# Optimization experiments

Hardware: AMD Instinct MI355X
Metric: run time of the kernel (lower is better)

The kernel has to match this reference:

```python
import jax, jax.numpy as jnp
import numpy as np

NUM_HEADS = 16
NUM_KV_HEADS = 4
HEAD_DIM = 128
TOP_K = 4
RMS_EPS = 1e-6
ROPE_THETA = 10000.0


def setup_inputs() -> dict:
    key = jax.random.key(0)
    ks = jax.random.split(key, 10)
    T, h, E, I, SI = 1024, 2048, 16, 512, 1024
    s = 0.02  # weight init scale for numerical sanity
    return {
        "hidden_states": jax.random.normal(ks[0], (T, h), jnp.float32),
        "residual": jax.random.normal(ks[1], (T, h), jnp.float32),
        "rms1_w": jnp.ones((h,), jnp.float32),
        "rms2_w": jnp.ones((h,), jnp.float32),
        "w_qkv": jax.random.normal(ks[2], (h, NUM_HEADS * HEAD_DIM + 2 * NUM_KV_HEADS * HEAD_DIM), jnp.float32) * s,
        "w_dense": jax.random.normal(ks[3], (NUM_HEADS * HEAD_DIM, h), jnp.float32) * s,
        "gate_w": jax.random.normal(ks[4], (h, E), jnp.float32) * s,
        "w13": jax.random.normal(ks[5], (E, h, 2 * I), jnp.float32) * s,
        "w2": jax.random.normal(ks[6], (E, I, h), jnp.float32) * s,
        "sw13": jax.random.normal(ks[7], (h, 2 * SI), jnp.float32) * s,
        "sw2": jax.random.normal(ks[8], (SI, h), jnp.float32) * s,
        "position_ids": jnp.arange(T, dtype=jnp.int32),
    }


def _rmsnorm(x, w, eps=RMS_EPS):
    var = jnp.mean(jnp.square(x), axis=-1, keepdims=True)
    return x * jax.lax.rsqrt(var + eps) * w


def _rope_neox(pos, x):
    # x: [T, H, D]; rotate-half (neox) style over full head_dim
    d = x.shape[-1]
    inv_freq = 1.0 / (ROPE_THETA ** (jnp.arange(0, d, 2, dtype=jnp.float32) / d))  # [d/2]
    ang = pos.astype(jnp.float32)[:, None] * inv_freq  # [T, d/2]
    cos = jnp.cos(ang)[:, None, :]  # [T, 1, d/2]
    sin = jnp.sin(ang)[:, None, :]
    x1, x2 = x[..., : d // 2], x[..., d // 2 :]
    return jnp.concatenate([x1 * cos - x2 * sin, x2 * cos + x1 * sin], axis=-1)


def reference(hidden_states, residual, rms1_w, rms2_w, w_qkv, w_dense,
              gate_w, w13, w2, sw13, sw2, position_ids):
    T, h = hidden_states.shape
    q_size = NUM_HEADS * HEAD_DIM
    kv_size = NUM_KV_HEADS * HEAD_DIM

    # --- input RMSNorm with fused residual add ---
    resid = hidden_states + residual
    x = _rmsnorm(resid, rms1_w)

    # --- attention ---
    qkv = x @ w_qkv
    q = qkv[:, :q_size].reshape(T, NUM_HEADS, HEAD_DIM)
    k = qkv[:, q_size : q_size + kv_size].reshape(T, NUM_KV_HEADS, HEAD_DIM)
    v = qkv[:, q_size + kv_size :].reshape(T, NUM_KV_HEADS, HEAD_DIM)
    q = _rope_neox(position_ids, q)
    k = _rope_neox(position_ids, k)
    rep = NUM_HEADS // NUM_KV_HEADS
    kr = jnp.repeat(k, rep, axis=1)  # [T, H, D]
    vr = jnp.repeat(v, rep, axis=1)
    scale = HEAD_DIM ** -0.5
    scores = jnp.einsum('thd,shd->hts', q, kr) * scale  # [H, T, T]
    causal = jnp.tril(jnp.ones((T, T), dtype=bool))
    scores = jnp.where(causal[None], scores, -1e9)
    probs = jax.nn.softmax(scores, axis=-1)
    ctx = jnp.einsum('hts,shd->thd', probs, vr).reshape(T, q_size)
    attn_out = ctx @ w_dense

    # --- post-attention RMSNorm with fused residual add ---
    resid2 = attn_out + resid
    x2 = _rmsnorm(resid2, rms2_w)

    # --- shared experts (SiLU-and-mul MLP) ---
    gu = x2 @ sw13
    sg, su = jnp.split(gu, 2, axis=-1)
    shared = (jax.nn.silu(sg) * su) @ sw2

    # --- MoE routing: softmax -> top-k -> renormalize ---
    E = gate_w.shape[1]
    router_probs = jax.nn.softmax(x2 @ gate_w, axis=-1)  # [T, E]
    topk_w, topk_ids = jax.lax.top_k(router_probs, TOP_K)
    topk_w = topk_w / jnp.sum(topk_w, axis=-1, keepdims=True)
    comb = jnp.zeros((T, E), x2.dtype).at[jnp.arange(T)[:, None], topk_ids].add(topk_w)

    # --- experts (dense grouped-GEMM equivalent, combined by routing weights) ---
    h_all = jnp.einsum('td,edf->etf', x2, w13)  # [E, T, 2I]
    eg, eu = jnp.split(h_all, 2, axis=-1)
    act = jax.nn.silu(eg) * eu  # [E, T, I]
    moe = jnp.einsum('etf,efh,te->th', act, w2, comb)

    return (moe + shared, resid2)
```

## Files before the change

### kernel.cpp

```cpp
#include <hip/hip_runtime.h>
#include <math.h>

#define HD 2048
#define NQH 16
#define NKVH 4
#define HEADD 128
#define QKVN 3072
#define NEXP 16
#define EI 512
#define SSI 1024
#define TOPK 4
#define TT 1024

typedef __bf16 bf16x8 __attribute__((ext_vector_type(8)));
typedef float f32x4 __attribute__((ext_vector_type(4)));

static __device__ __forceinline__ unsigned short f2bf(float f) {
    union { float f; unsigned int u; } v; v.f = f;
    unsigned int r = v.u + 0x7fff + ((v.u >> 16) & 1);
    return (unsigned short)(r >> 16);
}

static __device__ __forceinline__ void gl_lds16(const unsigned short* g,
                                                unsigned short* l) {
    __builtin_amdgcn_global_load_lds(
        (const __attribute__((address_space(1))) unsigned int*)g,
        (__attribute__((address_space(3))) unsigned int*)l, 16, 0, 0);
}

__global__ __launch_bounds__(256) void add_rmsnorm_kernel(
    const float* __restrict__ a, const float* __restrict__ b,
    const float* __restrict__ w, float* __restrict__ resid_out,
    unsigned short* __restrict__ x_bf)
{
    int t = blockIdx.x;
    int tid = threadIdx.x;
    const float4* a4 = (const float4*)(a + (size_t)t * HD);
    const float4* b4 = b ? (const float4*)(b + (size_t)t * HD) : nullptr;
    float4* r4 = resid_out ? (float4*)(resid_out + (size_t)t * HD) : nullptr;
    const float4* w4 = (const float4*)w;

    float4 v[2];
    float ss = 0.f;
#pragma unroll
    for (int l = 0; l < 2; ++l) {
        int idx = tid + l * 256;
        float4 va = a4[idx];
        if (b4) {
            float4 vb = b4[idx];
            va.x += vb.x; va.y += vb.y; va.z += vb.z; va.w += vb.w;
        }
        if (r4) r4[idx] = va;
        v[l] = va;
        ss += va.x * va.x + va.y * va.y + va.z * va.z + va.w * va.w;
    }
    for (int off = 32; off > 0; off >>= 1) ss += __shfl_down(ss, off);
    __shared__ float red[4];
    int lane = tid & 63, wv = tid >> 6;
    if (lane == 0) red[wv] = ss;
    __syncthreads();
    if (tid == 0) {
        float s = red[0] + red[1] + red[2] + red[3];
        red[0] = rsqrtf(s / (float)HD + 1e-6f);
    }
    __syncthreads();
    float inv = red[0];
#pragma unroll
    for (int l = 0; l < 2; ++l) {
        int idx = tid + l * 256;
        float4 va = v[l], vw = w4[idx];
        ushort4 ob;
        ob.x = f2bf(va.x * inv * vw.x);
        ob.y = f2bf(va.y * inv * vw.y);
        ob.z = f2bf(va.z * inv * vw.z);
        ob.w = f2bf(va.w * inv * vw.w);
        ((ushort4*)(x_bf + (size_t)t * HD))[idx] = ob;
    }
}

__global__ __launch_bounds__(256) void transpose_convert(
    const float* __restrict__ in, unsigned short* __restrict__ out,
    int K, int N, long long strideIn, long long strideOut)
{
    __shared__ float tile[32][33];
    const int n0 = blockIdx.x * 32;
    const int k0 = blockIdx.y * 32;
    const float* ip = in + (size_t)blockIdx.z * strideIn;
    unsigned short* op = out + (size_t)blockIdx.z * strideOut;
    int tid = threadIdx.x;
    int r = tid >> 3, c = (tid & 7) * 4;
    float4 v = *(const float4*)(ip + (size_t)(k0 + r) * N + n0 + c);
    tile[r][c] = v.x; tile[r][c + 1] = v.y; tile[r][c + 2] = v.z; tile[r][c + 3] = v.w;
    __syncthreads();
    ushort4 o;
    o.x = f2bf(tile[c + 0][r]);
    o.y = f2bf(tile[c + 1][r]);
    o.z = f2bf(tile[c + 2][r]);
    o.w = f2bf(tile[c + 3][r]);
    *(ushort4*)(op + (size_t)(n0 + r) * K + k0 + c) = o;
}

#define SBK 64

__global__ __launch_bounds__(256) void gemm_splitk(
    const unsigned short* __restrict__ A, const unsigned short* __restrict__ B,
    float* __restrict__ Cpart, int M, int N, int Kc, int ldA, int ldB)
{
    __shared__ unsigned short As[2][128 * SBK];
    __shared__ unsigned short Bs[2][128 * SBK];

    const int tid = threadIdx.x;
    const int wave = tid >> 6;
    const int lane = tid & 63;
    const int wr = wave >> 1, wc = wave & 1;
    const int l15 = lane & 15;
    const int row0 = blockIdx.y * 128;
    const int col0 = blockIdx.x * 128;
    const int z = blockIdx.z;

    const unsigned short* Ap = A + (size_t)row0 * ldA + (size_t)z * Kc;
    const unsigned short* Bp = B + (size_t)col0 * ldB + (size_t)z * Kc;

    const int r_st = tid >> 3;
    const int q_st = tid & 7;
    const int csrc = (q_st ^ (r_st & 7)) << 3;

    f32x4 acc[4][4] = {};

    const int nsteps = Kc / SBK;

#define STAGE_SK(buf, k0s)                                                    \
    {                                                                         \
        _Pragma("unroll")                                                     \
        for (int i = 0; i < 4; ++i) {                                         \
            int rr = r_st + i * 32;                                           \
            gl_lds16(Ap + (size_t)rr * ldA + (k0s) + csrc,                    \
                     &As[buf][rr * SBK + q_st * 8]);                          \
            gl_lds16(Bp + (size_t)rr * ldB + (k0s) + csrc,                    \
                     &Bs[buf][rr * SBK + q_st * 8]);                          \
        }                                                                     \
    }

    STAGE_SK(0, 0);

    for (int s = 0; s < nsteps; ++s) {
        const int cur = s & 1;
        if (s + 1 < nsteps) {
            STAGE_SK(cur ^ 1, (s + 1) * SBK);
            asm volatile("s_waitcnt vmcnt(8)" ::: "memory");
        } else {
            asm volatile("s_waitcnt vmcnt(0)" ::: "memory");
        }
        __builtin_amdgcn_s_barrier();

#pragma unroll
        for (int half = 0; half < 2; ++half) {
            const int q = half * 4 + (lane >> 4);
            bf16x8 af[4], bfv[4];
#pragma unroll
            for (int i = 0; i < 4; ++i) {
                int R = wr * 64 + i * 16 + l15;
                af[i] = *(const bf16x8*)&As[cur][R * SBK + ((q ^ (R & 7)) << 3)];
            }
#pragma unroll
            for (int j = 0; j < 4; ++j) {
                int R = wc * 64 + j * 16 + l15;
                bfv[j] = *(const bf16x8*)&Bs[cur][R * SBK + ((q ^ (R & 7)) << 3)];
            }
#pragma unroll
            for (int mi = 0; mi < 4; ++mi)
#pragma unroll
                for (int nj = 0; nj < 4; ++nj)
                    acc[mi][nj] = __builtin_amdgcn_mfma_f32_16x16x32_bf16(
                        af[mi], bfv[nj], acc[mi][nj], 0, 0, 0);
        }
        __builtin_amdgcn_s_barrier();
    }

    float* Cp = Cpart + (size_t)z * M * N;
#pragma unroll
    for (int mi = 0; mi < 4; ++mi)
#pragma unroll
        for (int nj = 0; nj < 4; ++nj)
#pragma unroll
            for (int r = 0; r < 4; ++r) {
                int row = row0 + wr * 64 + mi * 16 + (lane >> 4) * 4 + r;
                int col = col0 + wc * 64 + nj * 16 + l15;
                Cp[(size_t)row * N + col] = acc[mi][nj][r];
            }
}

__global__ __launch_bounds__(256) void reduce_partials(
    const float* __restrict__ part, int ns, int n4,
    const float* __restrict__ add, float* __restrict__ out, int acc)
{
    const float4* p4 = (const float4*)part;
    const float4* a4 = (const float4*)add;
    float4* o4 = (float4*)out;
    for (int idx = blockIdx.x * 256 + threadIdx.x; idx < n4;
         idx += gridDim.x * 256) {
        float4 s = p4[idx];
        for (int z = 1; z < ns; ++z) {
            float4 q = p4[(size_t)z * n4 + idx];
            s.x += q.x; s.y += q.y; s.z += q.z; s.w += q.w;
        }
        if (add) {
            float4 q = a4[idx];
            s.x += q.x; s.y += q.y; s.z += q.z; s.w += q.w;
        }
        if (acc) {
            float4 q = o4[idx];
            s.x += q.x; s.y += q.y; s.z += q.z; s.w += q.w;
        }
        o4[idx] = s;
    }
}

__global__ __launch_bounds__(256) void reduce_swiglu(
    const float* __restrict__ part, int ns, unsigned short* __restrict__ out)
{
    int idx4 = blockIdx.x * 256 + threadIdx.x;
    int t = idx4 >> 8;
    int i4 = (idx4 & 255) * 4;
    const float4* pg = (const float4*)(part + (size_t)t * (2 * SSI) + i4);
    const float4* pu = (const float4*)(part + (size_t)t * (2 * SSI) + SSI + i4);
    float4 g = pg[0], u = pu[0];
    for (int z = 1; z < ns; ++z) {
        float4 g2 = *(const float4*)((const float*)pg + (size_t)z * TT * 2 * SSI);
        float4 u2 = *(const float4*)((const float*)pu + (size_t)z * TT * 2 * SSI);
        g.x += g2.x; g.y += g2.y; g.z += g2.z; g.w += g2.w;
        u.x += u2.x; u.y += u2.y; u.z += u2.z; u.w += u2.w;
    }
    ushort4 o;
    o.x = f2bf((g.x / (1.f + __expf(-g.x))) * u.x);
    o.y = f2bf((g.y / (1.f + __expf(-g.y))) * u.y);
    o.z = f2bf((g.z / (1.f + __expf(-g.z))) * u.z);
    o.w = f2bf((g.w / (1.f + __expf(-g.w))) * u.w);
    *(ushort4*)(out + (size_t)t * SSI + i4) = o;
}

__global__ __launch_bounds__(256) void build_lists(
    const float* __restrict__ comb, int* __restrict__ lists,
    int* __restrict__ slots, int* __restrict__ cnts)
{
    int e = blockIdx.x;
    int tid = threadIdx.x;
    __shared__ int sc[256];
    int loc[4];
    int c = 0;
#pragma unroll
    for (int j = 0; j < 4; ++j) {
        int t = tid * 4 + j;
        if (comb[(size_t)t * NEXP + e] > 0.f) loc[c++] = t;
    }
    sc[tid] = c;
    __syncthreads();
    for (int off = 1; off < 256; off <<= 1) {
        int v = (tid >= off) ? sc[tid - off] : 0;
        __syncthreads();
        sc[tid] += v;
        __syncthreads();
    }
    int base = sc[tid] - c;
    for (int i = 0; i < c; ++i) {
        int t = loc[i];
        int s = 0;
        for (int e2 = 0; e2 < e; ++e2)
            s += (comb[(size_t)t * NEXP + e2] > 0.f) ? 1 : 0;
        lists[e * TT + base + i] = t;
        slots[e * TT + base + i] = s;
    }
    if (tid == 255) cnts[e] = sc[255];
}

__global__ void scan_cnts(const int* __restrict__ cnts, int* __restrict__ bases)
{
    if (threadIdx.x == 0 && blockIdx.x == 0) {
        int a = 0;
        for (int e = 0; e < NEXP; ++e) { bases[e] = a; a += cnts[e]; }
        bases[NEXP] = a;
    }
}

__global__ __launch_bounds__(256) void moe_up_gather(
    const unsigned short* __restrict__ x2B,
    const unsigned short* __restrict__ w13T,
    const float* __restrict__ comb,
    const int* __restrict__ lists,
    const int* __restrict__ cnts,
    const int* __restrict__ bases,
    unsigned short* __restrict__ actC)
{
    __shared__ unsigned short As[2][64 * 64];
    __shared__ unsigned short Bgs[2][64 * 64];
    __shared__ unsigned short Bus[2][64 * 64];

    const int e = blockIdx.z;
    const int cnt = cnts[e];
    const int m0 = blockIdx.y * 64;
    if (m0 >= cnt) return;
    const int n0 = blockIdx.x * 64;
    const int base_e = bases[e];

    const int tid = threadIdx.x;
    const int w = tid >> 6;
    const int lane = tid & 63;
    const int l15 = lane & 15;
    const int g = lane >> 4;

    const int r0 = tid >> 3;
    const int q_st = tid & 7;
    const int swz = (q_st ^ (r0 & 7)) << 3;

    int a0 = m0 + r0, a1 = m0 + r0 + 32;
    int tok0 = lists[e * TT + (a0 < cnt ? a0 : cnt - 1)];
    int tok1 = lists[e * TT + (a1 < cnt ? a1 : cnt - 1)];
    const unsigned short* Asrc0 = x2B + (size_t)tok0 * HD;
    const unsigned short* Asrc1 = x2B + (size_t)tok1 * HD;
    const unsigned short* Bbase = w13T + (size_t)e * 1024 * HD;
    const unsigned short* Bg0 = Bbase + (size_t)(n0 + r0) * HD;
    const unsigned short* Bg1 = Bbase + (size_t)(n0 + r0 + 32) * HD;
    const unsigned short* Bu0 = Bg0 + (size_t)512 * HD;
    const unsigned short* Bu1 = Bg1 + (size_t)512 * HD;

    f32x4 ag[4] = {};
    f32x4 au[4] = {};

#define STAGE_UP(buf, k0s)                                                    \
    {                                                                         \
        gl_lds16(Asrc0 + (k0s) + swz, &As[buf][(tid) * 8]);                   \
        gl_lds16(Asrc1 + (k0s) + swz, &As[buf][(tid + 256) * 8]);             \
        gl_lds16(Bg0 + (k0s) + swz, &Bgs[buf][(tid) * 8]);                    \
        gl_lds16(Bg1 + (k0s) + swz, &Bgs[buf][(tid + 256) * 8]);              \
        gl_lds16(Bu0 + (k0s) + swz, &Bus[buf][(tid) * 8]);                    \
        gl_lds16(Bu1 + (k0s) + swz, &Bus[buf][(tid + 256) * 8]);              \
    }

    STAGE_UP(0, 0);

    const int nsteps = HD / 64;
    for (int s = 0; s < nsteps; ++s) {
        const int cur = s & 1;
        if (s + 1 < nsteps) {
            STAGE_UP(cur ^ 1, (s + 1) * 64);
            asm volatile("s_waitcnt vmcnt(6)" ::: "memory");
        } else {
            asm volatile("s_waitcnt vmcnt(0)" ::: "memory");
        }
        __builtin_amdgcn_s_barrier();

#pragma unroll
        for (int kk2 = 0; kk2 < 2; ++kk2) {
            const int q = kk2 * 4 + g;
            bf16x8 af[4], bg, bu;
#pragma unroll
            for (int i = 0; i < 4; ++i) {
                int R = i * 16 + l15;
                af[i] = *(const bf16x8*)&As[cur][R * 64 + ((q ^ (R & 7)) << 3)];
            }
            {
                int R = w * 16 + l15;
                int off = R * 64 + ((q ^ (R & 7)) << 3);
                bg = *(const bf16x8*)&Bgs[cur][off];
                bu = *(const bf16x8*)&Bus[cur][off];
            }
#pragma unroll
            for (int mi = 0; mi < 4; ++mi) {
                ag[mi] = __builtin_amdgcn_mfma_f32_16x16x32_bf16(
                    af[mi], bg, ag[mi], 0, 0, 0);
                au[mi] = __builtin_amdgcn_mfma_f32_16x16x32_bf16(
                    af[mi], bu, au[mi], 0, 0, 0);
            }
        }
        __builtin_amdgcn_s_barrier();
    }

#pragma unroll
    for (int mi = 0; mi < 4; ++mi) {
#pragma unroll
        for (int r = 0; r < 4; ++r) {
            int grow = m0 + mi * 16 + g * 4 + r;
            if (grow >= cnt) continue;
            int tok = lists[e * TT + grow];
            float cw = comb[(size_t)tok * NEXP + e];
            int col = n0 + w * 16 + l15;
            float gg = ag[mi][r];
            float uu = au[mi][r];
            float v = (gg / (1.f + __expf(-gg))) * uu * cw;
            actC[(size_t)(base_e + grow) * EI + col] = f2bf(v);
        }
    }
}

__global__ __launch_bounds__(256) void moe_down_gather(
    const unsigned short* __restrict__ actC,
    const unsigned short* __restrict__ w2T,
    const int* __restrict__ lists,
    const int* __restrict__ slots,
    const int* __restrict__ cnts,
    const int* __restrict__ bases,
    float* __restrict__ slotpart)
{
    __shared__ unsigned short As[2][64 * 64];
    __shared__ unsigned short Bs[2][128 * 64];

    const int e = blockIdx.z;
    const int cnt = cnts[e];
    const int m0 = blockIdx.y * 64;
    if (m0 >= cnt) return;
    const int n0 = blockIdx.x * 128;
    const int base_e = bases[e];

    const int tid = threadIdx.x;
    const int w = tid >> 6;
    const int lane = tid & 63;
    const int l15 = lane & 15;
    const int g = lane >> 4;

    const int r0 = tid >> 3;
    const int q_st = tid & 7;
    const int swz = (q_st ^ (r0 & 7)) << 3;

    int a0 = m0 + r0, a1 = m0 + r0 + 32;
    const unsigned short* Asrc0 =
        actC + (size_t)(base_e + (a0 < cnt ? a0 : cnt - 1)) * EI;
    const unsigned short* Asrc1 =
        actC + (size_t)(base_e + (a1 < cnt ? a1 : cnt - 1)) * EI;
    const unsigned short* Bbase = w2T + (size_t)e * EI;

#define STAGE_DN(buf, k0s)                                                    \
    {                                                                         \
        gl_lds16(Asrc0 + (k0s) + swz, &As[buf][(tid) * 8]);                   \
        gl_lds16(Asrc1 + (k0s) + swz, &As[buf][(tid + 256) * 8]);             \
        _Pragma("unroll")                                                     \
        for (int i = 0; i < 4; ++i) {                                         \
            int rr = r0 + i * 32;                                             \
            gl_lds16(Bbase + (size_t)(n0 + rr) * (NEXP * EI) + (k0s) + swz,   \
                     &Bs[buf][(tid + i * 256) * 8]);                          \
        }                                                                     \
    }

    f32x4 acc[4][2] = {};

    STAGE_DN(0, 0);

    const int nsteps = EI / 64;
    for (int s = 0; s < nsteps; ++s) {
        const int cur = s & 1;
        if (s + 1 < nsteps) {
            STAGE_DN(cur ^ 1, (s + 1) * 64);
            asm volatile("s_waitcnt vmcnt(6)" ::: "memory");
        } else {
            asm volatile("s_waitcnt vmcnt(0)" ::: "memory");
        }
        __builtin_amdgcn_s_barrier();

#pragma unroll
        for (int kk2 = 0; kk2 < 2; ++kk2) {
            const int q = kk2 * 4 + g;
            bf16x8 af[4], bf[2];
#pragma unroll
            for (int i = 0; i < 4; ++i) {
                int R = i * 16 + l15;
                af[i] = *(const bf16x8*)&As[cur][R * 64 + ((q ^ (R & 7)) << 3)];
            }
#pragma unroll
            for (int j = 0; j < 2; ++j) {
                int R = w * 32 + j * 16 + l15;
                bf[j] = *(const bf16x8*)&Bs[cur][R * 64 + ((q ^ (R & 7)) << 3)];
            }
#pragma unroll
            for (int mi = 0; mi < 4; ++mi)
#pragma unroll
                for (int nj = 0; nj < 2; ++nj)
                    acc[mi][nj] = __builtin_amdgcn_mfma_f32_16x16x32_bf16(
                        af[mi], bf[nj], acc[mi][nj], 0, 0, 0);
        }
        __builtin_amdgcn_s_barrier();
    }

#pragma unroll
    for (int mi = 0; mi < 4; ++mi) {
#pragma unroll
        for (int r = 0; r < 4; ++r) {
            int grow = m0 + mi * 16 + g * 4 + r;
            if (grow >= cnt) continue;
            int tok = lists[e * TT + grow];
            int sl  = slots[e * TT + grow];
            float* orow = slotpart + (size_t)sl * TT * HD + (size_t)tok * HD;
#pragma unroll
            for (int nj = 0; nj < 2; ++nj) {
                int col = n0 + w * 32 + nj * 16 + l15;
                orow[col] = acc[mi][nj][r];
            }
        }
    }
}

__global__ __launch_bounds__(256) void rope_pack(
    const float* __restrict__ qkv, const int* __restrict__ pos_ids,
    unsigned short* __restrict__ Qb, unsigned short* __restrict__ Kb,
    unsigned short* __restrict__ Vb)
{
    const float SCALE = 0.08838834764831843f;
    int t = blockIdx.x;
    int tid = threadIdx.x;
    int w = tid >> 6, lane = tid & 63;
    float pos = (float)pos_ids[t];
    float invf = powf(10000.0f, -(float)lane * (1.0f / 64.0f));
    float ang = pos * invf;
    float c = cosf(ang);
    float s = sinf(ang);
    const float* row = qkv + (size_t)t * QKVN;
#pragma unroll
    for (int j = 0; j < 5; ++j) {
        int hh = w * 5 + j;
        const float* hb = row + hh * HEADD;
        float x1 = hb[lane], x2 = hb[lane + 64];
        float o1 = x1 * c - x2 * s;
        float o2 = x2 * c + x1 * s;
        if (hh < NQH) {
            unsigned short* qp = Qb + ((size_t)hh * TT + t) * HEADD;
            qp[lane] = f2bf(o1 * SCALE);
            qp[lane + 64] = f2bf(o2 * SCALE);
        } else {
            unsigned short* kp = Kb + ((size_t)(hh - NQH) * TT + t) * HEADD;
            kp[lane] = f2bf(o1);
            kp[lane + 64] = f2bf(o2);
        }
    }
    float2 v2 = *(const float2*)(row + 2560 + tid * 2);
    int kvh = tid >> 6;
    int d = (tid * 2) & 127;
    unsigned int packed = (unsigned int)f2bf(v2.x) |
                          ((unsigned int)f2bf(v2.y) << 16);
    *(unsigned int*)(Vb + ((size_t)kvh * TT + t) * HEADD + d) = packed;
}

__global__ __launch_bounds__(256) void transpose_v(
    const unsigned short* __restrict__ Vb, unsigned short* __restrict__ Vt)
{
    __shared__ unsigned short tile[32][40];
    const int kvh = blockIdx.z;
    const int t0 = blockIdx.x * 32, d0 = blockIdx.y * 32;
    int tid = threadIdx.x;
    int r = tid >> 3, c4 = (tid & 7) * 4;
    ushort4 v = *(const ushort4*)(Vb + ((size_t)kvh * TT + t0 + r) * HEADD + d0 + c4);
    tile[r][c4] = v.x; tile[r][c4 + 1] = v.y;
    tile[r][c4 + 2] = v.z; tile[r][c4 + 3] = v.w;
    __syncthreads();
    ushort4 o;
    o.x = tile[c4 + 0][r];
    o.y = tile[c4 + 1][r];
    o.z = tile[c4 + 2][r];
    o.w = tile[c4 + 3][r];
    *(ushort4*)(Vt + ((size_t)kvh * HEADD + d0 + r) * TT + t0 + c4) = o;
}

__global__ __launch_bounds__(128) void flash_attn_mfma(
    const unsigned short* __restrict__ Qb,
    const unsigned short* __restrict__ Kb,
    const unsigned short* __restrict__ Vt,
    unsigned short* __restrict__ ctx)
{
    __shared__ __align__(16) unsigned short Ks[2][64 * 128];
    __shared__ __align__(16) unsigned short Vs[2][128 * 64];
    __shared__ __align__(16) unsigned short Pl[2][16][72];

    const int h   = blockIdx.x;
    const int p   = blockIdx.y;
    const int rh  = blockIdx.z;
    const int kvh = h >> 2;
    const int tid = threadIdx.x;
    const int w   = tid >> 6;
    const int lane = tid & 63;
    const int l15 = lane & 15;
    const int g   = lane >> 4;

    const unsigned short* Kh = Kb + (size_t)kvh * TT * HEADD;
    const unsigned short* Vh = Vt + (size_t)kvh * HEADD * TT;

#define STAGE_KV(buf, s0s)                                                    \
    {                                                                         \
        _Pragma("unroll")                                                     \
        for (int i = 0; i < 8; ++i) {                                         \
            int idx = tid + i * 128;                                          \
            int r = idx >> 4, c = idx & 15;                                   \
            int csw = (c & 8) | ((c ^ r) & 7);                                \
            gl_lds16(Kh + (size_t)((s0s) + r) * HEADD + csw * 8,              \
                     &Ks[buf][idx * 8]);                                      \
        }                                                                     \
        _Pragma("unroll")                                                     \
        for (int i = 0; i < 8; ++i) {                                         \
            int idx = tid + i * 128;                                          \
            int r = idx >> 3, c = idx & 7;                                    \
            int csw = (c ^ r) & 7;                                            \
            gl_lds16(Vh + (size_t)r * TT + (s0s) + csw * 8,                   \
                     &Vs[buf][idx * 8]);                                      \
        }                                                                     \
    }

    const int qts[2] = {p, 15 - p};

#pragma unroll
    for (int qi = 0; qi < 2; ++qi) {
        const int qt = qts[qi];
        const int q0 = qt * 64 + rh * 32 + w * 16;
        const int ntiles = qt + 1;

        const unsigned short* Qrow = Qb + ((size_t)h * TT + q0 + l15) * HEADD;
        bf16x8 qf[4];
#pragma unroll
        for (int kk = 0; kk < 4; ++kk)
            qf[kk] = *(const bf16x8*)(Qrow + kk * 32 + g * 8);

        float m_i[4], l_i[4];
#pragma unroll
        for (int r = 0; r < 4; ++r) { m_i[r] = -1e30f; l_i[r] = 0.f; }
        f32x4 of[8] = {};

        STAGE_KV(0, 0);

        for (int st = 0; st < ntiles; ++st) {
            const int cur = st & 1;
            const int s0 = st * 64;
            if (st + 1 < ntiles) {
                STAGE_KV(cur ^ 1, (st + 1) * 64);
                asm volatile("s_waitcnt vmcnt(16)" ::: "memory");
            } else {
                asm volatile("s_waitcnt vmcnt(0)" ::: "memory");
            }
            __builtin_amdgcn_s_barrier();

            f32x4 sacc[4] = {};
#pragma unroll
            for (int kk = 0; kk < 4; ++kk) {
#pragma unroll
                for (int n = 0; n < 4; ++n) {
                    int R = n * 16 + l15;
                    int cidx = kk * 4 + g;
                    int cs = (cidx & 8) | ((cidx ^ R) & 7);
                    bf16x8 kb = *(const bf16x8*)&Ks[cur][R * 128 + cs * 8];
                    sacc[n] = __builtin_amdgcn_mfma_f32_16x16x32_bf16(
                        qf[kk], kb, sacc[n], 0, 0, 0);
                }
            }

            const bool diag = (st == qt);
            float alpha[4];
#pragma unroll
            for (int r = 0; r < 4; ++r) {
                const int qrow = q0 + g * 4 + r;
                float sv[4] = {sacc[0][r], sacc[1][r], sacc[2][r], sacc[3][r]};
                if (diag) {
#pragma unroll
                    for (int n = 0; n < 4; ++n)
                        if (s0 + n * 16 + l15 > qrow) sv[n] = -1e30f;
                }
                float rm = fmaxf(fmaxf(sv[0], sv[1]), fmaxf(sv[2], sv[3]));
                rm = fmaxf(rm, __shfl_xor(rm, 1));
                rm = fmaxf(rm, __shfl_xor(rm, 2));
                rm = fmaxf(rm, __shfl_xor(rm, 4));
                rm = fmaxf(rm, __shfl_xor(rm, 8));
                float mnew = fmaxf(m_i[r], rm);
                alpha[r] = __expf(m_i[r] - mnew);
                float p0 = __expf(sv[0] - mnew);
                float p1 = __expf(sv[1] - mnew);
                float p2 = __expf(sv[2] - mnew);
                float p3 = __expf(sv[3] - mnew);
                float rs = p0 + p1 + p2 + p3;
                rs += __shfl_xor(rs, 1);
                rs += __shfl_xor(rs, 2);
                rs += __shfl_xor(rs, 4);
                rs += __shfl_xor(rs, 8);
                l_i[r] = l_i[r] * alpha[r] + rs;
                m_i[r] = mnew;
                Pl[w][g * 4 + r][0 * 16 + l15] = f2bf(p0);
                Pl[w][g * 4 + r][1 * 16 + l15] = f2bf(p1);
                Pl[w][g * 4 + r][2 * 16 + l15] = f2bf(p2);
                Pl[w][g * 4 + r][3 * 16 + l15] = f2bf(p3);
            }

#pragma unroll
            for (int nd = 0; nd < 8; ++nd)
#pragma unroll
                for (int r = 0; r < 4; ++r)
                    of[nd][r] *= alpha[r];

#pragma unroll
            for (int kk2 = 0; kk2 < 2; ++kk2) {
                bf16x8 pa = *(const bf16x8*)&Pl[w][l15][kk2 * 32 + g * 8];
#pragma unroll
                for (int nd = 0; nd < 8; ++nd) {
                    int R = nd * 16 + l15;
                    int cidx = kk2 * 4 + g;
                    int cs = (cidx ^ R) & 7;
                    bf16x8 vb = *(const bf16x8*)&Vs[cur][R * 64 + cs * 8];
                    of[nd] = __builtin_amdgcn_mfma_f32_16x16x32_bf16(
                        pa, vb, of[nd], 0, 0, 0);
                }
            }
            __builtin_amdgcn_s_barrier();
        }

        float invl[4];
#pragma unroll
        for (int r = 0; r < 4; ++r) invl[r] = 1.f / l_i[r];
#pragma unroll
        for (int nd = 0; nd < 8; ++nd)
#pragma unroll
            for (int r = 0; r < 4; ++r) {
                int trow = q0 + g * 4 + r;
                ctx[(size_t)trow * (NQH * HEADD) + h * HEADD + nd * 16 + l15] =
                    f2bf(of[nd][r] * invl[r]);
            }
    }
}

__global__ __launch_bounds__(256) void router_fused(
    const float* __restrict__ resid2, const float* __restrict__ w,
    const float* __restrict__ gate_w, float* __restrict__ comb)
{
    int t = blockIdx.x;
    int tid = threadIdx.x;
    int lane = tid & 63, wv = tid >> 6;

    const float4* r4 = (const float4*)(resid2 + (size_t)t * HD);
    float4 xa = r4[tid * 2], xb = r4[tid * 2 + 1];
    float ss = xa.x * xa.x + xa.y * xa.y + xa.z * xa.z + xa.w * xa.w +
               xb.x * xb.x + xb.y * xb.y + xb.z * xb.z + xb.w * xb.w;
    for (int off = 32; off > 0; off >>= 1) ss += __shfl_down(ss, off);
    __shared__ float red[4];
    if (lane == 0) red[wv] = ss;
    __syncthreads();
    float inv = rsqrtf((red[0] + red[1] + red[2] + red[3]) / (float)HD + 1e-6f);

    const float4* w4 = (const float4*)w;
    float4 wa = w4[tid * 2], wb = w4[tid * 2 + 1];
    float xs[8] = {xa.x * wa.x * inv, xa.y * wa.y * inv, xa.z * wa.z * inv,
                   xa.w * wa.w * inv, xb.x * wb.x * inv, xb.y * wb.y * inv,
                   xb.z * wb.z * inv, xb.w * wb.w * inv};

    float acc[16] = {};
    int kbase = tid * 8;
#pragma unroll
    for (int j = 0; j < 8; ++j) {
        float xv = xs[j];
        const float4* wrow = (const float4*)(gate_w + (size_t)(kbase + j) * NEXP);
        float4 w0 = wrow[0], w1 = wrow[1], w2 = wrow[2], w3 = wrow[3];
        acc[0] += xv * w0.x;  acc[1] += xv * w0.y;  acc[2] += xv * w0.z;  acc[3] += xv * w0.w;
        acc[4] += xv * w1.x;  acc[5] += xv * w1.y;  acc[6] += xv * w1.z;  acc[7] += xv * w1.w;
        acc[8] += xv * w2.x;  acc[9] += xv * w2.y;  acc[10] += xv * w2.z; acc[11] += xv * w2.w;
        acc[12] += xv * w3.x; acc[13] += xv * w3.y; acc[14] += xv * w3.z; acc[15] += xv * w3.w;
    }
    __shared__ float red2[4][16];
#pragma unroll
    for (int e = 0; e < 16; ++e) {
        float v = acc[e];
        v += __shfl_xor(v, 1);
        v += __shfl_xor(v, 2);
        v += __shfl_xor(v, 4);
        v += __shfl_xor(v, 8);
        v += __shfl_xor(v, 16);
        v += __shfl_xor(v, 32);
        if (lane == 0) red2[wv][e] = v;
    }
    __syncthreads();

    if (tid == 0) {
        float l[NEXP];
#pragma unroll
        for (int e = 0; e < NEXP; ++e)
            l[e] = red2[0][e] + red2[1][e] + red2[2][e] + red2[3][e];
        int sel[TOPK];
        float selv[TOPK];
        bool used[NEXP] = {};
#pragma unroll
        for (int r = 0; r < TOPK; ++r) {
            int best = -1;
            float bv = -1e30f;
            for (int e = 0; e < NEXP; ++e)
                if (!used[e] && l[e] > bv) { bv = l[e]; best = e; }
            used[best] = true;
            sel[r] = best;
            selv[r] = bv;
        }
        float mx = selv[0];
        float wsum = 0.f, wvv[TOPK];
#pragma unroll
        for (int r = 0; r < TOPK; ++r) { wvv[r] = __expf(selv[r] - mx); wsum += wvv[r]; }
        float out16[NEXP] = {};
#pragma unroll
        for (int r = 0; r < TOPK; ++r) out16[sel[r]] = wvv[r] / wsum;
#pragma unroll
        for (int e = 0; e < NEXP; ++e) comb[(size_t)t * NEXP + e] = out16[e];
    }
}

extern "C" void kernel_launch(void* const* d_in, const int* in_sizes, int n_in,
                              void* d_out, int out_size, void* d_ws, size_t ws_size,
                              hipStream_t stream)
{
    const float* hidden   = (const float*)d_in[0];
    const float* residual = (const float*)d_in[1];
    const float* rms1_w   = (const float*)d_in[2];
    const float* rms2_w   = (const float*)d_in[3];
    const float* w_qkv    = (const float*)d_in[4];
    const float* w_dense  = (const float*)d_in[5];
    const float* gate_w   = (const float*)d_in[6];
    const float* w13      = (const float*)d_in[7];
    const float* w2       = (const float*)d_in[8];
    const float* sw13     = (const float*)d_in[9];
    const float* sw2      = (const float*)d_in[10];
    const int*   pos_ids  = (const int*)d_in[11];

    const int T = TT;

    float* out0 = (float*)d_out;
    float* out1 = (float*)d_out + (size_t)T * HD;

    char* base = (char*)d_ws;
    float*          residF = (float*)(base);
    unsigned short* xB     = (unsigned short*)(base + 8388608);
    unsigned short* ctxB   = (unsigned short*)(base + 12582912);
    unsigned short* actC   = (unsigned short*)(base);
    float*          qkvF   = (float*)(base + 16777216);
    unsigned short* x2B    = (unsigned short*)(base + 29360128);
    unsigned short* sactB  = (unsigned short*)(base + 33554432);
    float*          comb   = (float*)(base + 35651584);
    float*          part   = (float*)(base + 35717120);
    unsigned short* Wbuf   = (unsigned short*)(base + 69271552);
    int*            lists  = (int*)(base + 139526144);
    int*            cnts   = (int*)(base + 139591680);
    int*            slots  = (int*)(base + 139591936);
    int*            bases  = (int*)(base + 139657472);

    unsigned short* Qb = (unsigned short*)(base + 35717120);
    unsigned short* Kb = Qb + (size_t)NQH * TT * HEADD;
    unsigned short* Vb = Kb + (size_t)NKVH * TT * HEADD;
    unsigned short* Vt = Vb + (size_t)NKVH * TT * HEADD;

    dim3 blk(256);

    add_rmsnorm_kernel<<<dim3(T), blk, 0, stream>>>(
        hidden, residual, rms1_w, residF, xB);

    transpose_convert<<<dim3(QKVN / 32, HD / 32), blk, 0, stream>>>(
        w_qkv, Wbuf, HD, QKVN, 0, 0);
    gemm_splitk<<<dim3(QKVN / 128, T / 128, 2), blk, 0, stream>>>(
        xB, Wbuf, part, T, QKVN, 1024, HD, HD);
    reduce_partials<<<dim3(1024), blk, 0, stream>>>(
        part, 2, T * QKVN / 4, nullptr, qkvF, 0);

    rope_pack<<<dim3(T), blk, 0, stream>>>(qkvF, pos_ids, Qb, Kb, Vb);
    transpose_v<<<dim3(T / 32, HEADD / 32, NKVH), blk, 0, stream>>>(Vb, Vt);

    flash_attn_mfma<<<dim3(NQH, 8, 2), dim3(128), 0, stream>>>(Qb, Kb, Vt, ctxB);

    transpose_convert<<<dim3(HD / 32, HD / 32), blk, 0, stream>>>(
        w_dense, Wbuf, HD, HD, 0, 0);
    gemm_splitk<<<dim3(HD / 128, T / 128, 4), blk, 0, stream>>>(
        ctxB, Wbuf, part, T, HD, 512, HD, HD);
    reduce_partials<<<dim3(1024), blk, 0, stream>>>(
        part, 4, T * HD / 4, residF, out1, 0);

    add_rmsnorm_kernel<<<dim3(T), blk, 0, stream>>>(
        out1, nullptr, rms2_w, nullptr, x2B);

    router_fused<<<dim3(T), blk, 0, stream>>>(out1, rms2_w, gate_w, comb);
    build_lists<<<dim3(NEXP), blk, 0, stream>>>(comb, lists, slots, cnts);
    scan_cnts<<<dim3(1), dim3(64), 0, stream>>>(cnts, bases);

    transpose_convert<<<dim3(HD / 32, HD / 32), blk, 0, stream>>>(
        sw13, Wbuf, HD, 2 * SSI, 0, 0);
    gemm_splitk<<<dim3(HD / 128, T / 128, 4), blk, 0, stream>>>(
        x2B, Wbuf, part, T, 2 * SSI, 512, HD, HD);

    reduce_swiglu<<<dim3(T * SSI / 4 / 256), blk, 0, stream>>>(part, 4, sactB);

    transpose_convert<<<dim3(HD / 32, SSI / 32), blk, 0, stream>>>(
        sw2, Wbuf, SSI, HD, 0, 0);
    gemm_splitk<<<dim3(HD / 128, T / 128, 4), blk, 0, stream>>>(
        sactB, Wbuf, part, T, HD, 256, SSI, SSI);
    reduce_partials<<<dim3(1024), blk, 0, stream>>>(
        part, 4, T * HD / 4, nullptr, out0, 0);

    transpose_convert<<<dim3(1024 / 32, HD / 32, NEXP), blk, 0, stream>>>(
        w13, Wbuf, HD, 1024, (long long)HD * 1024, (long long)1024 * HD);
    moe_up_gather<<<dim3(EI / 64, 16, NEXP), blk, 0, stream>>>(
        x2B, Wbuf, comb, lists, cnts, bases, actC);

    transpose_convert<<<dim3(HD / 32, (NEXP * EI) / 32), blk, 0, stream>>>(
        w2, Wbuf, NEXP * EI, HD, 0, 0);
    moe_down_gather<<<dim3(HD / 128, 16, NEXP), blk, 0, stream>>>(
        actC, Wbuf, lists, slots, cnts, bases, part);
    reduce_partials<<<dim3(1024), blk, 0, stream>>>(
        part, 4, T * HD / 4, nullptr, out0, 1);
}
```

Baseline: 360.3 us.

## Triple-buffer MoE GEMMs, widen weight transpose tiles, fuse QKV split-K reduce into RoPE

Moves the MoE up and down gather GEMMs from double- to triple-buffered LDS staging, keeping two K-steps of global loads in flight to hide memory latency. The weight transpose/convert kernel now handles 64-row K tiles per block and writes 16-byte bf16 vectors, halving its block count. The QKV split-K reduce kernel is dropped and rope_pack sums the two partial buffers directly, removing one full fp32 round trip. Tripling LDS use in the MoE kernels may lower occupancy, and the transpose grid for sw13 was also corrected to match its shape.

```diff
diff --git a/kernel.cpp b/kernel.cpp
--- a/kernel.cpp
+++ b/kernel.cpp
@@ -14,6 +14,7 @@
 
 typedef __bf16 bf16x8 __attribute__((ext_vector_type(8)));
 typedef float f32x4 __attribute__((ext_vector_type(4)));
+typedef unsigned short u16x8 __attribute__((ext_vector_type(8)));
 
 static __device__ __forceinline__ unsigned short f2bf(float f) {
     union { float f; unsigned int u; } v; v.f = f;
@@ -82,22 +83,27 @@
     const float* __restrict__ in, unsigned short* __restrict__ out,
     int K, int N, long long strideIn, long long strideOut)
 {
-    __shared__ float tile[32][33];
+    __shared__ float tile[64][33];
     const int n0 = blockIdx.x * 32;
-    const int k0 = blockIdx.y * 32;
+    const int k0 = blockIdx.y * 64;
     const float* ip = in + (size_t)blockIdx.z * strideIn;
     unsigned short* op = out + (size_t)blockIdx.z * strideOut;
     int tid = threadIdx.x;
-    int r = tid >> 3, c = (tid & 7) * 4;
-    float4 v = *(const float4*)(ip + (size_t)(k0 + r) * N + n0 + c);
-    tile[r][c] = v.x; tile[r][c + 1] = v.y; tile[r][c + 2] = v.z; tile[r][c + 3] = v.w;
+    int c = (tid & 7) * 4;
+#pragma unroll
+    for (int i = 0; i < 2; ++i) {
+        int r = (tid >> 3) + i * 32;
+        float4 v = *(const float4*)(ip + (size_t)(k0 + r) * N + n0 + c);
+        tile[r][c] = v.x; tile[r][c + 1] = v.y;
+        tile[r][c + 2] = v.z; tile[r][c + 3] = v.w;
+    }
     __syncthreads();
-    ushort4 o;
-    o.x = f2bf(tile[c + 0][r]);
-    o.y = f2bf(tile[c + 1][r]);
-    o.z = f2bf(tile[c + 2][r]);
-    o.w = f2bf(tile[c + 3][r]);
-    *(ushort4*)(op + (size_t)(n0 + r) * K + k0 + c) = o;
+    int rr = tid >> 3;
+    int kc = (tid & 7) * 8;
+    u16x8 o;
+#pragma unroll
+    for (int j = 0; j < 8; ++j) o[j] = f2bf(tile[kc + j][rr]);
+    *(u16x8*)(op + (size_t)(n0 + rr) * K + k0 + kc) = o;
 }
 
 #define SBK 64
@@ -291,9 +297,9 @@
     const int* __restrict__ bases,
     unsigned short* __restrict__ actC)
 {
-    __shared__ unsigned short As[2][64 * 64];
-    __shared__ unsigned short Bgs[2][64 * 64];
-    __shared__ unsigned short Bus[2][64 * 64];
+    __shared__ unsigned short As[3][64 * 64];
+    __shared__ unsigned short Bgs[3][64 * 64];
+    __shared__ unsigned short Bus[3][64 * 64];
 
     const int e = blockIdx.z;
     const int cnt = cnts[e];
@@ -336,13 +342,16 @@
         gl_lds16(Bu1 + (k0s) + swz, &Bus[buf][(tid + 256) * 8]);              \
     }
 
+    const int nsteps = HD / 64;
     STAGE_UP(0, 0);
-
-    const int nsteps = HD / 64;
+    STAGE_UP(1, 64);
+
     for (int s = 0; s < nsteps; ++s) {
-        const int cur = s & 1;
-        if (s + 1 < nsteps) {
-            STAGE_UP(cur ^ 1, (s + 1) * 64);
+        const int cur = s % 3;
+        if (s + 2 < nsteps) {
+            STAGE_UP((s + 2) % 3, (s + 2) * 64);
+            asm volatile("s_waitcnt vmcnt(12)" ::: "memory");
+        } else if (s + 1 < nsteps) {
             asm volatile("s_waitcnt vmcnt(6)" ::: "memory");
         } else {
             asm volatile("s_waitcnt vmcnt(0)" ::: "memory");
@@ -401,8 +410,8 @@
     const int* __restrict__ bases,
     float* __restrict__ slotpart)
 {
-    __shared__ unsigned short As[2][64 * 64];
-    __shared__ unsigned short Bs[2][128 * 64];
+    __shared__ unsigned short As[3][64 * 64];
+    __shared__ unsigned short Bs[3][128 * 64];
 
     const int e = blockIdx.z;
     const int cnt = cnts[e];
@@ -442,13 +451,16 @@
 
     f32x4 acc[4][2] = {};
 
+    const int nsteps = EI / 64;
     STAGE_DN(0, 0);
-
-    const int nsteps = EI / 64;
+    STAGE_DN(1, 64);
+
     for (int s = 0; s < nsteps; ++s) {
-        const int cur = s & 1;
-        if (s + 1 < nsteps) {
-            STAGE_DN(cur ^ 1, (s + 1) * 64);
+        const int cur = s % 3;
+        if (s + 2 < nsteps) {
+            STAGE_DN((s + 2) % 3, (s + 2) * 64);
+            asm volatile("s_waitcnt vmcnt(12)" ::: "memory");
+        } else if (s + 1 < nsteps) {
             asm volatile("s_waitcnt vmcnt(6)" ::: "memory");
         } else {
             asm volatile("s_waitcnt vmcnt(0)" ::: "memory");
@@ -498,7 +510,8 @@
 }
 
 __global__ __launch_bounds__(256) void rope_pack(
-    const float* __restrict__ qkv, const int* __restrict__ pos_ids,
+    const float* __restrict__ qkv0, const float* __restrict__ qkv1,
+    const int* __restrict__ pos_ids,
     unsigned short* __restrict__ Qb, unsigned short* __restrict__ Kb,
     unsigned short* __restrict__ Vb)
 {
@@ -511,12 +524,15 @@
     float ang = pos * invf;
     float c = cosf(ang);
     float s = sinf(ang);
-    const float* row = qkv + (size_t)t * QKVN;
+    const float* row0 = qkv0 + (size_t)t * QKVN;
+    const float* row1 = qkv1 + (size_t)t * QKVN;
 #pragma unroll
     for (int j = 0; j < 5; ++j) {
         int hh = w * 5 + j;
-        const float* hb = row + hh * HEADD;
-        float x1 = hb[lane], x2 = hb[lane + 64];
+        const float* hb0 = row0 + hh * HEADD;
+        const float* hb1 = row1 + hh * HEADD;
+        float x1 = hb0[lane] + hb1[lane];
+        float x2 = hb0[lane + 64] + hb1[lane + 64];
         float o1 = x1 * c - x2 * s;
         float o2 = x2 * c + x1 * s;
         if (hh < NQH) {
@@ -529,11 +545,12 @@
             kp[lane + 64] = f2bf(o2);
         }
     }
-    float2 v2 = *(const float2*)(row + 2560 + tid * 2);
+    float2 v0 = *(const float2*)(row0 + 2560 + tid * 2);
+    float2 v1 = *(const float2*)(row1 + 2560 + tid * 2);
     int kvh = tid >> 6;
     int d = (tid * 2) & 127;
-    unsigned int packed = (unsigned int)f2bf(v2.x) |
-                          ((unsigned int)f2bf(v2.y) << 16);
+    unsigned int packed = (unsigned int)f2bf(v0.x + v1.x) |
+                          ((unsigned int)f2bf(v0.y + v1.y) << 16);
     *(unsigned int*)(Vb + ((size_t)kvh * TT + t) * HEADD + d) = packed;
 }
 
@@ -824,7 +841,6 @@
     unsigned short* xB     = (unsigned short*)(base + 8388608);
     unsigned short* ctxB   = (unsigned short*)(base + 12582912);
     unsigned short* actC   = (unsigned short*)(base);
-    float*          qkvF   = (float*)(base + 16777216);
     unsigned short* x2B    = (unsigned short*)(base + 29360128);
     unsigned short* sactB  = (unsigned short*)(base + 33554432);
     float*          comb   = (float*)(base + 35651584);
@@ -835,7 +851,7 @@
     int*            slots  = (int*)(base + 139591936);
     int*            bases  = (int*)(base + 139657472);
 
-    unsigned short* Qb = (unsigned short*)(base + 35717120);
+    unsigned short* Qb = (unsigned short*)(base + 35717120 + 25165824);
     unsigned short* Kb = Qb + (size_t)NQH * TT * HEADD;
     unsigned short* Vb = Kb + (size_t)NKVH * TT * HEADD;
     unsigned short* Vt = Vb + (size_t)NKVH * TT * HEADD;
@@ -845,19 +861,18 @@
     add_rmsnorm_kernel<<<dim3(T), blk, 0, stream>>>(
         hidden, residual, rms1_w, residF, xB);
 
-    transpose_convert<<<dim3(QKVN / 32, HD / 32), blk, 0, stream>>>(
+    transpose_convert<<<dim3(QKVN / 32, HD / 64), blk, 0, stream>>>(
         w_qkv, Wbuf, HD, QKVN, 0, 0);
     gemm_splitk<<<dim3(QKVN / 128, T / 128, 2), blk, 0, stream>>>(
         xB, Wbuf, part, T, QKVN, 1024, HD, HD);
-    reduce_partials<<<dim3(1024), blk, 0, stream>>>(
-        part, 2, T * QKVN / 4, nullptr, qkvF, 0);
-
-    rope_pack<<<dim3(T), blk, 0, stream>>>(qkvF, pos_ids, Qb, Kb, Vb);
+
+    rope_pack<<<dim3(T), blk, 0, stream>>>(
+        part, part + (size_t)T * QKVN, pos_ids, Qb, Kb, Vb);
     transpose_v<<<dim3(T / 32, HEADD / 32, NKVH), blk, 0, stream>>>(Vb, Vt);
 
     flash_attn_mfma<<<dim3(NQH, 8, 2), dim3(128), 0, stream>>>(Qb, Kb, Vt, ctxB);
 
-    transpose_convert<<<dim3(HD / 32, HD / 32), blk, 0, stream>>>(
+    transpose_convert<<<dim3(HD / 32, HD / 64), blk, 0, stream>>>(
         w_dense, Wbuf, HD, HD, 0, 0);
     gemm_splitk<<<dim3(HD / 128, T / 128, 4), blk, 0, stream>>>(
         ctxB, Wbuf, part, T, HD, 512, HD, HD);
@@ -871,26 +886,26 @@
     build_lists<<<dim3(NEXP), blk, 0, stream>>>(comb, lists, slots, cnts);
     scan_cnts<<<dim3(1), dim3(64), 0, stream>>>(cnts, bases);
 
-    transpose_convert<<<dim3(HD / 32, HD / 32), blk, 0, stream>>>(
+    transpose_convert<<<dim3(2 * SSI / 32, HD / 64), blk, 0, stream>>>(
         sw13, Wbuf, HD, 2 * SSI, 0, 0);
     gemm_splitk<<<dim3(HD / 128, T / 128, 4), blk, 0, stream>>>(
         x2B, Wbuf, part, T, 2 * SSI, 512, HD, HD);
 
     reduce_swiglu<<<dim3(T * SSI / 4 / 256), blk, 0, stream>>>(part, 4, sactB);
 
-    transpose_convert<<<dim3(HD / 32, SSI / 32), blk, 0, stream>>>(
+    transpose_convert<<<dim3(HD / 32, SSI / 64), blk, 0, stream>>>(
         sw2, Wbuf, SSI, HD, 0, 0);
     gemm_splitk<<<dim3(HD / 128, T / 128, 4), blk, 0, stream>>>(
         sactB, Wbuf, part, T, HD, 256, SSI, SSI);
     reduce_partials<<<dim3(1024), blk, 0, stream>>>(
         part, 4, T * HD / 4, nullptr, out0, 0);
 
-    transpose_convert<<<dim3(1024 / 32, HD / 32, NEXP), blk, 0, stream>>>(
+    transpose_convert<<<dim3(1024 / 32, HD / 64, NEXP), blk, 0, stream>>>(
         w13, Wbuf, HD, 1024, (long long)HD * 1024, (long long)1024 * HD);
     moe_up_gather<<<dim3(EI / 64, 16, NEXP), blk, 0, stream>>>(
         x2B, Wbuf, comb, lists, cnts, bases, actC);
 
-    transpose_convert<<<dim3(HD / 32, (NEXP * EI) / 32), blk, 0, stream>>>(
+    transpose_convert<<<dim3(HD / 32, (NEXP * EI) / 64), blk, 0, stream>>>(
         w2, Wbuf, NEXP * EI, HD, 0, 0);
     moe_down_gather<<<dim3(HD / 128, 16, NEXP), blk, 0, stream>>>(
         actC, Wbuf, lists, slots, cnts, bases, part);
```

Result: slower. 367.9 us (+2.1%).
